# Kernel tuning notes

Hardware: AMD Instinct MI355X
Metric: run time of the kernel (lower is better)

Reference implementation:

```python
import jax, jax.numpy as jnp
import numpy as np


def silu(v):
    return v * jax.nn.sigmoid(v)


def setup_inputs() -> dict:
    key = jax.random.key(0)
    ks = jax.random.split(key, 9)
    B, L, d_model = 2, 2048, 1024
    expand, d_state, d_conv = 2, 16, 4
    d_inner = expand * d_model          # 2048
    dt_rank = (d_model + 15) // 16      # 64 (ceil(d_model/16))
    sc = 0.02
    s = lambda k, shape: (jax.random.normal(k, shape, jnp.float32) * sc)
    A_init = jnp.tile(jnp.arange(1, d_state + 1, dtype=jnp.float32), (d_inner, 1))
    return {
        "x": jax.random.normal(ks[0], (B, L, d_model), jnp.float32),
        "in_proj_w": s(ks[1], (2 * d_inner, d_model)),
        "conv_w": s(ks[2], (d_inner, 1, d_conv)),
        "conv_b": s(ks[3], (d_inner,)),
        "x_proj_w": s(ks[4], (dt_rank + 2 * d_state, d_inner)),
        "dt_proj_w": s(ks[5], (d_inner, dt_rank)),
        "dt_proj_b": s(ks[6], (d_inner,)),
        "A_log": jnp.log(A_init),
        "D": jnp.ones((d_inner,), jnp.float32),
        "out_proj_w": s(ks[7], (d_model, d_inner)),
    }


def _mamba(x, in_proj_w, conv_w, conv_b, x_proj_w, dt_proj_w, dt_proj_b, A_log, D, out_proj_w):
    Bsz, L, d_model = x.shape
    d_inner, _, d_conv = conv_w.shape
    d_state = A_log.shape[1]
    dt_rank = dt_proj_w.shape[1]

    # input projection -> [B, L, 2*d_inner], split into conv branch and gate
    xz = jnp.einsum('bld,ed->ble', x, in_proj_w)
    x_in, z = jnp.split(xz, 2, axis=-1)

    # causal depthwise conv1d over sequence
    xt = jnp.transpose(x_in, (0, 2, 1))                      # [B, d_inner, L]
    xt = jnp.pad(xt, ((0, 0), (0, 0), (d_conv - 1, 0)))
    xc = jax.lax.conv_general_dilated(
        xt, conv_w, window_strides=(1,), padding='VALID',
        dimension_numbers=('NCH', 'OIH', 'NCH'),
        feature_group_count=d_inner)
    xc = xc + conv_b[None, :, None]
    u = silu(jnp.transpose(xc, (0, 2, 1)))                   # [B, L, d_inner]

    # ssm parameter projections
    x_dbl = jnp.einsum('ble,fe->blf', u, x_proj_w)           # [B, L, dt_rank + 2*d_state]
    dt, B_ssm, C_ssm = jnp.split(x_dbl, [dt_rank, dt_rank + d_state], axis=-1)
    delta = jax.nn.softplus(jnp.einsum('blr,er->ble', dt, dt_proj_w) + dt_proj_b)  # [B,L,d_inner]
    A = -jnp.exp(A_log)                                       # [d_inner, d_state]

    # selective scan: h_t = exp(delta_t * A) * h_{t-1} + delta_t * u_t * B_t
    def step(h, inp):
        d_t, B_t, C_t, u_t = inp                              # [B,e],[B,n],[B,n],[B,e]
        dA = jnp.exp(d_t[..., None] * A)                      # [B, d_inner, d_state]
        h = dA * h + (d_t * u_t)[..., None] * B_t[:, None, :]
        y = jnp.einsum('ben,bn->be', h, C_t)
        return h, y

    h0 = jnp.zeros((Bsz, d_inner, d_state), x.dtype)
    scan_in = (jnp.swapaxes(delta, 0, 1), jnp.swapaxes(B_ssm, 0, 1),
               jnp.swapaxes(C_ssm, 0, 1), jnp.swapaxes(u, 0, 1))
    _, ys = jax.lax.scan(step, h0, scan_in)                   # ys: [L, B, d_inner]
    y = jnp.swapaxes(ys, 0, 1) + u * D                        # skip term D*u

    y = y * silu(z)                                           # gate
    return jnp.einsum('ble,de->bld', y, out_proj_w)


def reference(x, in_proj_w, conv_w, conv_b, x_proj_w, dt_proj_w, dt_proj_b, A_log, D, out_proj_w):
    # ResidualMamba: x + Mamba(x)
    return x + _mamba(x, in_proj_w, conv_w, conv_b, x_proj_w,
                      dt_proj_w, dt_proj_b, A_log, D, out_proj_w)
```

## Files before the change

### kernel.cpp

```cpp
#include <hip/hip_runtime.h>
#include <hip/hip_bf16.h>
#include <math.h>

typedef __bf16 bf16;
typedef __attribute__((ext_vector_type(8))) __bf16 bf16x8;
typedef __attribute__((ext_vector_type(4))) __bf16 bf16x4;
typedef __attribute__((ext_vector_type(4))) float  f32x4;

static constexpr int Bsz = 2, L = 2048, DM = 1024, DI = 2048, DS = 16, DTR = 64;
static constexpr int M   = Bsz * L;
static constexpr int NXZ = 2 * DI;
static constexpr int NXD = DTR + 2 * DS;
static constexpr int NC  = 32;
static constexpr int CL  = L / NC;
static constexpr int KS  = 8;
static constexpr float LOG2E = 1.4426950408889634f;

__device__ inline float ex2(float x) { return __builtin_amdgcn_exp2f(x); }

static constexpr int C0 = M * DM / 4;
static constexpr int C1 = C0 + NXZ * DM / 4;
static constexpr int C2 = C1 + DM * DI / 4;
static constexpr int C3 = C2 + NXD * DI / 4;
static constexpr int C4 = C3 + DI * DTR / 4;

__global__ __launch_bounds__(256)
void cast_all(const float* __restrict__ s0, const float* __restrict__ s1,
              const float* __restrict__ s2, const float* __restrict__ s3,
              const float* __restrict__ s4,
              bf16* __restrict__ d0, bf16* __restrict__ d1,
              bf16* __restrict__ d2, bf16* __restrict__ d3,
              bf16* __restrict__ d4)
{
    const int i = blockIdx.x * 256 + threadIdx.x;
    const float* s; bf16* d; int off;
    if      (i < C0) { s = s0; d = d0; off = 0;  }
    else if (i < C1) { s = s1; d = d1; off = C0; }
    else if (i < C2) { s = s2; d = d2; off = C1; }
    else if (i < C3) { s = s3; d = d3; off = C2; }
    else             { s = s4; d = d4; off = C3; }
    const int j = i - off;
    float4 v = ((const float4*)s)[j];
    bf16x4 o = {(bf16)v.x, (bf16)v.y, (bf16)v.z, (bf16)v.w};
    ((bf16x4*)d)[j] = o;
}

__device__ inline void gload_lds16(const void* g, void* l)
{
    __builtin_amdgcn_global_load_lds(
        (const __attribute__((address_space(1))) void*)g,
        (__attribute__((address_space(3))) void*)l, 16, 0, 0);
}

template<int EPI>
__global__ __launch_bounds__(256)
void gemm_bf16(const bf16* __restrict__ A, const bf16* __restrict__ Bw,
               const float* __restrict__ bias, const float* __restrict__ res,
               void* __restrict__ Cout, int N, int K, int lda, int ldc)
{
    __shared__ __align__(16) bf16 Asl[128 * 32];
    __shared__ __align__(16) bf16 Bsl[128 * 32];

    const int tid  = threadIdx.x;
    const int row0 = blockIdx.y * 128;
    const int col0 = blockIdx.x * 128;
    const int w    = tid >> 6;
    const int lane = tid & 63;
    const int wr   = w >> 1, wc = w & 1;
    const int fr   = lane & 15;
    const int ko   = (lane >> 4) << 3;

    f32x4 acc[4][4] = {};

    const int sr = tid >> 2;
    const int sk = (tid & 3) << 3;
    int brow0 = col0 + sr;       if (brow0 > N - 1) brow0 = N - 1;
    int brow1 = col0 + 64 + sr;  if (brow1 > N - 1) brow1 = N - 1;
    const bf16* gA0 = A  + (size_t)(row0 + sr) * lda + sk;
    const bf16* gA1 = A  + (size_t)(row0 + 64 + sr) * lda + sk;
    const bf16* gB0 = Bw + (size_t)brow0 * K + sk;
    const bf16* gB1 = Bw + (size_t)brow1 * K + sk;
    char* lA = (char*)Asl + w * 1024;
    char* lB = (char*)Bsl + w * 1024;

    for (int k0 = 0; k0 < K; k0 += 32) {
        gload_lds16(gA0 + k0, lA);
        gload_lds16(gA1 + k0, lA + 4096);
        gload_lds16(gB0 + k0, lB);
        gload_lds16(gB1 + k0, lB + 4096);
        __syncthreads();

        bf16x8 af[4], bfr[4];
#pragma unroll
        for (int m = 0; m < 4; ++m)
            af[m] = *(const bf16x8*)&Asl[((wr << 6) + m * 16 + fr) * 32 + ko];
#pragma unroll
        for (int n = 0; n < 4; ++n)
            bfr[n] = *(const bf16x8*)&Bsl[((wc << 6) + n * 16 + fr) * 32 + ko];
#pragma unroll
        for (int m = 0; m < 4; ++m)
#pragma unroll
            for (int n = 0; n < 4; ++n)
                acc[m][n] = __builtin_amdgcn_mfma_f32_16x16x32_bf16(
                    af[m], bfr[n], acc[m][n], 0, 0, 0);
        __syncthreads();
    }

    const int r0 = row0 + (wr << 6) + ((lane >> 4) << 2);
    const int c0 = col0 + (wc << 6) + fr;
#pragma unroll
    for (int m = 0; m < 4; ++m) {
#pragma unroll
        for (int n = 0; n < 4; ++n) {
            const int col = c0 + n * 16;
            if (col < N) {
#pragma unroll
                for (int r = 0; r < 4; ++r) {
                    const int row = r0 + m * 16 + r;
                    float v = acc[m][n][r];
                    if (EPI == 0) {
                        ((bf16*)Cout)[(size_t)row * ldc + col] = (bf16)v;
                    } else if (EPI == 1) {
                        v += bias[col];
                        v = (v > 20.f) ? v : log1pf(expf(v));
                        ((bf16*)Cout)[(size_t)row * ldc + col] = (bf16)v;
                    } else {
                        ((float*)Cout)[(size_t)row * ldc + col] =
                            v + res[(size_t)row * ldc + col];
                    }
                }
            }
        }
    }
}

__global__ __launch_bounds__(256)
void gemm_xproj(const bf16* __restrict__ A, const bf16* __restrict__ Bw,
                float* __restrict__ Cpart)
{
    __shared__ __align__(16) bf16 Asl[128 * 32];
    __shared__ __align__(16) bf16 Bsl[128 * 32];

    const int tid  = threadIdx.x;
    const int row0 = blockIdx.x * 128;
    const int kz   = blockIdx.y;
    const int kb   = kz * (2048 / KS);
    const int w    = tid >> 6;
    const int lane = tid & 63;
    const int wr   = w >> 1, wc = w & 1;
    const int fr   = lane & 15;
    const int ko   = (lane >> 4) << 3;

    f32x4 acc[4][4] = {};

    const int sr = tid >> 2;
    const int sk = (tid & 3) << 3;
    int brow0 = sr;       if (brow0 > 95) brow0 = 95;
    int brow1 = 64 + sr;  if (brow1 > 95) brow1 = 95;
    const bf16* gA0 = A  + (size_t)(row0 + sr) * DI + kb + sk;
    const bf16* gA1 = A  + (size_t)(row0 + 64 + sr) * DI + kb + sk;
    const bf16* gB0 = Bw + (size_t)brow0 * DI + kb + sk;
    const bf16* gB1 = Bw + (size_t)brow1 * DI + kb + sk;
    char* lA = (char*)Asl + w * 1024;
    char* lB = (char*)Bsl + w * 1024;

    for (int k0 = 0; k0 < 2048 / KS; k0 += 32) {
        gload_lds16(gA0 + k0, lA);
        gload_lds16(gA1 + k0, lA + 4096);
        gload_lds16(gB0 + k0, lB);
        gload_lds16(gB1 + k0, lB + 4096);
        __syncthreads();

        bf16x8 af[4], bfr[4];
#pragma unroll
        for (int m = 0; m < 4; ++m)
            af[m] = *(const bf16x8*)&Asl[((wr << 6) + m * 16 + fr) * 32 + ko];
#pragma unroll
        for (int n = 0; n < 4; ++n)
            bfr[n] = *(const bf16x8*)&Bsl[((wc << 6) + n * 16 + fr) * 32 + ko];
#pragma unroll
        for (int m = 0; m < 4; ++m)
#pragma unroll
            for (int n = 0; n < 4; ++n)
                acc[m][n] = __builtin_amdgcn_mfma_f32_16x16x32_bf16(
                    af[m], bfr[n], acc[m][n], 0, 0, 0);
        __syncthreads();
    }

    const int r0 = (wr << 6) + ((lane >> 4) << 2);
    const int c0 = (wc << 6) + fr;
    float* Cp = Cpart + (size_t)kz * M * 96 + (size_t)row0 * 96;
#pragma unroll
    for (int m = 0; m < 4; ++m) {
#pragma unroll
        for (int n = 0; n < 4; ++n) {
            const int col = c0 + n * 16;
            if (col < 96) {
#pragma unroll
                for (int r = 0; r < 4; ++r)
                    Cp[(size_t)(r0 + m * 16 + r) * 96 + col] = acc[m][n][r];
            }
        }
    }
}

__global__ __launch_bounds__(256)
void reduce_xdbl(const float* __restrict__ part, bf16* __restrict__ xdb)
{
    const int i = blockIdx.x * 256 + threadIdx.x;
    if (i >= M * 96) return;
    float s = 0.f;
#pragma unroll
    for (int k = 0; k < KS; ++k) s += part[(size_t)k * M * 96 + i];
    xdb[i] = (bf16)s;
}

__global__ __launch_bounds__(256)
void conv_silu(const bf16* __restrict__ xzb, const float* __restrict__ cw,
               const float* __restrict__ cb, bf16* __restrict__ u)
{
    const int idx = blockIdx.x * 256 + threadIdx.x;
    const int e   = (idx & 255) * 8;
    const int m   = idx >> 8;
    const int l   = m & (L - 1);

    float wv[8][4];
#pragma unroll
    for (int c = 0; c < 8; ++c) {
        float4 t = *(const float4*)(cw + (size_t)(e + c) * 4);
        wv[c][0] = t.x; wv[c][1] = t.y; wv[c][2] = t.z; wv[c][3] = t.w;
    }
    float acc[8];
    {
        float4 b0 = *(const float4*)(cb + e);
        float4 b1 = *(const float4*)(cb + e + 4);
        acc[0] = b0.x; acc[1] = b0.y; acc[2] = b0.z; acc[3] = b0.w;
        acc[4] = b1.x; acc[5] = b1.y; acc[6] = b1.z; acc[7] = b1.w;
    }
#pragma unroll
    for (int k = 0; k < 4; ++k) {
        if (l + k - 3 >= 0) {
            bf16x8 xv = *(const bf16x8*)&xzb[(size_t)(m + k - 3) * NXZ + e];
#pragma unroll
            for (int c = 0; c < 8; ++c)
                acc[c] = fmaf((float)xv[c], wv[c][k], acc[c]);
        }
    }
    bf16x8 o;
#pragma unroll
    for (int c = 0; c < 8; ++c)
        o[c] = (bf16)(acc[c] / (1.f + __expf(-acc[c])));
    *(bf16x8*)&u[(size_t)m * DI + e] = o;
}

__global__ __launch_bounds__(256)
void scan_pass1(const bf16* __restrict__ xzb, const bf16* __restrict__ ub,
                const bf16* __restrict__ xdb, const float* __restrict__ A_log,
                float* __restrict__ Pend, float* __restrict__ Qend)
{
    __shared__ bf16 sD[CL][256];
    __shared__ bf16 sU[CL][256];
    __shared__ float Bs[CL][DS];
    const int tid = threadIdx.x;
    const int e0 = blockIdx.x * 256;
    const int e  = e0 + tid;
    const int c = blockIdx.y;
    const int b = blockIdx.z;
    const int l0 = c * CL;

#pragma unroll
    for (int it = 0; it < CL / 8; ++it) {
        const int r   = it * 8 + (tid >> 5);
        const int col = (tid & 31) * 8;
        *(bf16x8*)&sD[r][col] = *(const bf16x8*)&xzb[(size_t)(b * L + l0 + r) * NXZ + e0 + col];
        *(bf16x8*)&sU[r][col] = *(const bf16x8*)&ub [(size_t)(b * L + l0 + r) * DI  + e0 + col];
    }
#pragma unroll
    for (int it = 0; it < CL * DS / 256; ++it) {
        const int idx = it * 256 + tid;
        Bs[idx >> 4][idx & 15] =
            (float)xdb[(size_t)(b * L + l0 + (idx >> 4)) * NXD + DTR + (idx & 15)];
    }

    float A2[DS];
#pragma unroll
    for (int q = 0; q < 4; ++q) {
        float4 al = *(const float4*)(A_log + (size_t)e * DS + q * 4);
        A2[q * 4 + 0] = -__expf(al.x) * LOG2E;
        A2[q * 4 + 1] = -__expf(al.y) * LOG2E;
        A2[q * 4 + 2] = -__expf(al.z) * LOG2E;
        A2[q * 4 + 3] = -__expf(al.w) * LOG2E;
    }

    float h[DS];
#pragma unroll
    for (int n = 0; n < DS; ++n) h[n] = 0.f;
    float sumd = 0.f;

    __syncthreads();

#pragma unroll 4
    for (int t = 0; t < CL; ++t) {
        const float dv = (float)sD[t][tid];
        const float uv = (float)sU[t][tid];
        const float du = dv * uv;
        sumd += dv;
#pragma unroll
        for (int n = 0; n < DS; ++n) {
            const float a = ex2(dv * A2[n]);
            h[n] = fmaf(a, h[n], du * Bs[t][n]);
        }
    }

    const size_t o = ((size_t)(c * Bsz + b) * DI + e) * DS;
#pragma unroll
    for (int q = 0; q < 4; ++q) {
        f32x4 P = {ex2(A2[q*4] * sumd), ex2(A2[q*4+1] * sumd),
                   ex2(A2[q*4+2] * sumd), ex2(A2[q*4+3] * sumd)};
        *(f32x4*)(Pend + o + q * 4) = P;
        *(float4*)(Qend + o + q * 4) = make_float4(h[q*4], h[q*4+1], h[q*4+2], h[q*4+3]);
    }
}

__global__ __launch_bounds__(256)
void scan_pass2(const float* __restrict__ Pend, const float* __restrict__ Qend,
                float* __restrict__ H0)
{
    const int g = blockIdx.x * 256 + threadIdx.x;
    const int stride = Bsz * DI * DS;
    float P[NC], Q[NC];
#pragma unroll
    for (int c = 0; c < NC; ++c) {
        P[c] = Pend[(size_t)c * stride + g];
        Q[c] = Qend[(size_t)c * stride + g];
    }
    float h = 0.f;
#pragma unroll
    for (int c = 0; c < NC; ++c) {
        H0[(size_t)c * stride + g] = h;
        h = fmaf(P[c], h, Q[c]);
    }
}

__global__ __launch_bounds__(256)
void scan_pass3(bf16* __restrict__ xzb, const bf16* __restrict__ ub,
                const bf16* __restrict__ xdb, const float* __restrict__ A_log,
                const float* __restrict__ Dp, const float* __restrict__ H0)
{
    __shared__ bf16 sD[CL][256];
    __shared__ bf16 sU[CL][256];
    __shared__ float BCs[CL][2 * DS];
    const int tid = threadIdx.x;
    const int e0 = blockIdx.x * 256;
    const int e  = e0 + tid;
    const int c = blockIdx.y;
    const int b = blockIdx.z;
    const int l0 = c * CL;

#pragma unroll
    for (int it = 0; it < CL / 8; ++it) {
        const int r   = it * 8 + (tid >> 5);
        const int col = (tid & 31) * 8;
        const size_t grow = (size_t)(b * L + l0 + r);
        *(bf16x8*)&sD[r][col] = *(const bf16x8*)&xzb[grow * NXZ + e0 + col];
        *(bf16x8*)&sU[r][col] = *(const bf16x8*)&ub [grow * DI + e0 + col];
    }
#pragma unroll
    for (int it = 0; it < CL * 2 * DS / 256; ++it) {
        const int idx = it * 256 + tid;
        BCs[idx >> 5][idx & 31] =
            (float)xdb[(size_t)(b * L + l0 + (idx >> 5)) * NXD + DTR + (idx & 31)];
    }

    float A2[DS];
#pragma unroll
    for (int q = 0; q < 4; ++q) {
        float4 al = *(const float4*)(A_log + (size_t)e * DS + q * 4);
        A2[q * 4 + 0] = -__expf(al.x) * LOG2E;
        A2[q * 4 + 1] = -__expf(al.y) * LOG2E;
        A2[q * 4 + 2] = -__expf(al.z) * LOG2E;
        A2[q * 4 + 3] = -__expf(al.w) * LOG2E;
    }

    float h[DS];
    const size_t o = (size_t)c * (Bsz * DI * DS) + ((size_t)b * DI + e) * DS;
#pragma unroll
    for (int q = 0; q < 4; ++q) {
        float4 hv = *(const float4*)(H0 + o + q * 4);
        h[q*4] = hv.x; h[q*4+1] = hv.y; h[q*4+2] = hv.z; h[q*4+3] = hv.w;
    }
    const float Dval = Dp[e];

    __syncthreads();

#pragma unroll 4
    for (int t = 0; t < CL; ++t) {
        const float dv = (float)sD[t][tid];
        const float uv = (float)sU[t][tid];
        const float du = dv * uv;
        float y = 0.f;
#pragma unroll
        for (int n = 0; n < DS; ++n) {
            const float a = ex2(dv * A2[n]);
            h[n] = fmaf(a, h[n], du * BCs[t][n]);
            y = fmaf(h[n], BCs[t][DS + n], y);
        }
        sD[t][tid] = (bf16)(y + uv * Dval);
    }

    __syncthreads();
#pragma unroll
    for (int it = 0; it < CL / 8; ++it) {
        const int r   = it * 8 + (tid >> 5);
        const int col = (tid & 31) * 8;
        const size_t grow = (size_t)(b * L + l0 + r);
        bf16x8 zv = *(const bf16x8*)&xzb[grow * NXZ + DI + e0 + col];
        bf16x8 yv = *(bf16x8*)&sD[r][col];
        bf16x8 ov;
#pragma unroll
        for (int j = 0; j < 8; ++j) {
            const float z = (float)zv[j];
            ov[j] = (bf16)((float)yv[j] * (z / (1.f + __expf(-z))));
        }
        *(bf16x8*)&xzb[grow * NXZ + e0 + col] = ov;
    }
}

extern "C" void kernel_launch(void* const* d_in, const int* in_sizes, int n_in,
                              void* d_out, int out_size, void* d_ws, size_t ws_size,
                              hipStream_t stream)
{
    const float* x          = (const float*)d_in[0];
    const float* in_proj_w  = (const float*)d_in[1];
    const float* conv_w     = (const float*)d_in[2];
    const float* conv_b     = (const float*)d_in[3];
    const float* x_proj_w   = (const float*)d_in[4];
    const float* dt_proj_w  = (const float*)d_in[5];
    const float* dt_proj_b  = (const float*)d_in[6];
    const float* A_log      = (const float*)d_in[7];
    const float* Dp         = (const float*)d_in[8];
    const float* out_proj_w = (const float*)d_in[9];
    float* out = (float*)d_out;

    bf16* xzb   = (bf16*)d_ws;
    bf16* ub    = xzb   + (size_t)M * NXZ;
    bf16* xdb   = ub    + (size_t)M * DI;
    bf16* xb    = xdb   + (size_t)M * NXD;
    bf16* wbin  = xb    + (size_t)M * DM;
    bf16* wbout = wbin  + (size_t)NXZ * DM;
    bf16* wbxp  = wbout + (size_t)DM * DI;
    bf16* wbdt  = wbxp  + (size_t)NXD * DI;
    float* Pend = (float*)(wbdt + (size_t)DI * DTR);
    float* Qend = Pend + (size_t)NC * Bsz * DI * DS;
    float* H0   = Qend + (size_t)NC * Bsz * DI * DS;
    float* xpart = Pend;

    const dim3 blk(256);

    cast_all<<<dim3(C4 / 256), blk, 0, stream>>>(
        x, in_proj_w, out_proj_w, x_proj_w, dt_proj_w,
        xb, wbin, wbout, wbxp, wbdt);

    gemm_bf16<0><<<dim3(NXZ / 128, M / 128), blk, 0, stream>>>(
        xb, wbin, nullptr, nullptr, xzb, NXZ, DM, DM, NXZ);

    conv_silu<<<dim3(M * (DI / 8) / 256), blk, 0, stream>>>(xzb, conv_w, conv_b, ub);

    gemm_xproj<<<dim3(M / 128, KS), blk, 0, stream>>>(ub, wbxp, xpart);
    reduce_xdbl<<<dim3(M * 96 / 256), blk, 0, stream>>>(xpart, xdb);

    gemm_bf16<1><<<dim3(DI / 128, M / 128), blk, 0, stream>>>(
        xdb, wbdt, dt_proj_b, nullptr, xzb, DI, DTR, NXD, NXZ);

    scan_pass1<<<dim3(DI / 256, NC, Bsz), blk, 0, stream>>>(xzb, ub, xdb, A_log, Pend, Qend);
    scan_pass2<<<dim3(Bsz * DI * DS / 256), blk, 0, stream>>>(Pend, Qend, H0);
    scan_pass3<<<dim3(DI / 256, NC, Bsz), blk, 0, stream>>>(xzb, ub, xdb, A_log, Dp, H0);

    gemm_bf16<2><<<dim3(DM / 128, M / 128), blk, 0, stream>>>(
        xzb, wbout, nullptr, x, out, DM, DI, NXZ, DM);
}
```

Baseline: 274.5 us.

## Add 256x256 tiled multi-stage pipelined GEMM for the input projection

Replaces the generic 128x128 bf16 GEMM for the input projection with a dedicated 512-thread kernel. It uses 256x256 tiles, a 4-slot LDS ring buffer filled by direct global-to-LDS loads, XOR-swizzled LDS layout, interleaved prefetch with MFMA phases, s_setprio, and XCD-aware block remapping. The goal is more operand reuse per tile and hiding load latency on the largest GEMM. The cost is one block per CU with heavy register and LDS use, and a hand-tuned waitcnt/barrier schedule that is fragile.

```diff
diff --git a/kernel.cpp b/kernel.cpp
--- a/kernel.cpp
+++ b/kernel.cpp
@@ -17,6 +17,17 @@
 static constexpr float LOG2E = 1.4426950408889634f;
 
 __device__ inline float ex2(float x) { return __builtin_amdgcn_exp2f(x); }
+
+__device__ inline void gload_lds16(const void* g, void* l)
+{
+    __builtin_amdgcn_global_load_lds(
+        (const __attribute__((address_space(1))) void*)g,
+        (__attribute__((address_space(3))) void*)l, 16, 0, 0);
+}
+
+#define SBAR() { asm volatile("" ::: "memory"); __builtin_amdgcn_s_barrier(); asm volatile("" ::: "memory"); }
+#define VMCNT4() asm volatile("s_waitcnt vmcnt(4)" ::: "memory")
+#define VMCNT0() asm volatile("s_waitcnt vmcnt(0)" ::: "memory")
 
 static constexpr int C0 = M * DM / 4;
 static constexpr int C1 = C0 + NXZ * DM / 4;
@@ -45,11 +56,142 @@
     ((bf16x4*)d)[j] = o;
 }
 
-__device__ inline void gload_lds16(const void* g, void* l)
-{
-    __builtin_amdgcn_global_load_lds(
-        (const __attribute__((address_space(1))) void*)g,
-        (__attribute__((address_space(3))) void*)l, 16, 0, 0);
+static constexpr int GK  = DM;
+static constexpr int GNT = GK / 64;
+
+__device__ __forceinline__ void stage_half(const bf16* __restrict__ Gbase, int ld,
+                                           int kbase, bf16* lds_slot, int tid, int wid)
+{
+    const int rl = tid >> 2;
+    const int ks = ((tid & 3) ^ (rl & 3)) << 3;
+#pragma unroll
+    for (int i = 0; i < 2; ++i)
+        gload_lds16(Gbase + (size_t)(i * 128 + rl) * ld + kbase + ks,
+                    lds_slot + i * 4096 + wid * 512);
+}
+
+template<int MH>
+__device__ __forceinline__ void ldA4(const bf16* As, int abase, bf16x8 af[4])
+{
+#pragma unroll
+    for (int mm = 0; mm < 4; ++mm)
+        af[mm] = *(const bf16x8*)(As + abase + (MH * 4 + mm) * 512);
+}
+
+__device__ __forceinline__ void ldB4(const bf16* Bs, int bbase, bf16x8 bfr[4])
+{
+#pragma unroll
+    for (int nn = 0; nn < 4; ++nn)
+        bfr[nn] = *(const bf16x8*)(Bs + bbase + nn * 512);
+}
+
+template<int MH>
+__device__ __forceinline__ void mfma16(f32x4 acc[8][4], const bf16x8 af[4],
+                                       const bf16x8 bfr[4])
+{
+#pragma unroll
+    for (int mm = 0; mm < 4; ++mm)
+#pragma unroll
+        for (int nn = 0; nn < 4; ++nn)
+            acc[MH * 4 + mm][nn] = __builtin_amdgcn_mfma_f32_16x16x32_bf16(
+                af[mm], bfr[nn], acc[MH * 4 + mm][nn], 0, 0, 0);
+}
+
+__global__ __launch_bounds__(512, 1)
+void gemm256_inproj(const bf16* __restrict__ A, const bf16* __restrict__ Bw,
+                    bf16* __restrict__ C)
+{
+    __shared__ __align__(16) bf16 Asl[4 * 8192];
+    __shared__ __align__(16) bf16 Bsl[4 * 8192];
+
+    const int tid  = threadIdx.x;
+    const int wid  = tid >> 6;
+    const int lane = tid & 63;
+    const int wr   = wid >> 2;
+    const int wc   = wid & 3;
+    const int fr   = lane & 15;
+    const int ko16 = lane >> 4;
+    const int kx   = ((ko16 ^ (fr & 3)) << 3);
+
+    const int bid = blockIdx.x;
+    const int wg  = (bid & 7) * 32 + (bid >> 3);
+    const int by  = wg >> 4, bx = wg & 15;
+    const int row0 = by * 256, col0 = bx * 256;
+
+    const bf16* Ablk = A  + (size_t)row0 * GK;
+    const bf16* Bblk = Bw + (size_t)col0 * GK;
+
+    const int abase = (wr * 128 + fr) * 32 + kx;
+    const int bbase = (wc * 64 + fr) * 32 + kx;
+
+    f32x4 acc[8][4] = {};
+    bf16x8 af[4], bfr[4];
+
+    stage_half(Ablk, GK, 0,       Asl + 0 * 8192, tid, wid);
+    stage_half(Bblk, GK, 0,       Bsl + 0 * 8192, tid, wid);
+    stage_half(Ablk, GK, 32,      Asl + 1 * 8192, tid, wid);
+    stage_half(Bblk, GK, 32,      Bsl + 1 * 8192, tid, wid);
+    stage_half(Ablk, GK, 64,      Asl + 2 * 8192, tid, wid);
+    stage_half(Bblk, GK, 64,      Bsl + 2 * 8192, tid, wid);
+    VMCNT4();
+    SBAR();
+
+    for (int t = 0; t < GNT; ++t) {
+        const int sk0 = (2 * t) & 3, sk1 = (2 * t + 1) & 3;
+        const bf16* As0 = Asl + sk0 * 8192;
+        const bf16* As1 = Asl + sk1 * 8192;
+        const bf16* Bs0 = Bsl + sk0 * 8192;
+        const bf16* Bs1 = Bsl + sk1 * 8192;
+
+        ldA4<0>(As0, abase, af);
+        ldB4(Bs0, bbase, bfr);
+        if (t + 1 < GNT)
+            stage_half(Ablk, GK, (t + 1) * 64 + 32, Asl + ((2 * t + 3) & 3) * 8192, tid, wid);
+        SBAR();
+        __builtin_amdgcn_s_setprio(1);
+        mfma16<0>(acc, af, bfr);
+        __builtin_amdgcn_s_setprio(0);
+        SBAR();
+
+        ldA4<1>(As0, abase, af);
+        if (t + 1 < GNT)
+            stage_half(Bblk, GK, (t + 1) * 64 + 32, Bsl + ((2 * t + 3) & 3) * 8192, tid, wid);
+        SBAR();
+        __builtin_amdgcn_s_setprio(1);
+        mfma16<1>(acc, af, bfr);
+        __builtin_amdgcn_s_setprio(0);
+        SBAR();
+
+        ldA4<0>(As1, abase, af);
+        ldB4(Bs1, bbase, bfr);
+        if (t + 2 < GNT)
+            stage_half(Ablk, GK, (t + 2) * 64, Asl + sk0 * 8192, tid, wid);
+        SBAR();
+        __builtin_amdgcn_s_setprio(1);
+        mfma16<0>(acc, af, bfr);
+        __builtin_amdgcn_s_setprio(0);
+        SBAR();
+
+        ldA4<1>(As1, abase, af);
+        if (t + 2 < GNT)
+            stage_half(Bblk, GK, (t + 2) * 64, Bsl + sk0 * 8192, tid, wid);
+        SBAR();
+        __builtin_amdgcn_s_setprio(1);
+        mfma16<1>(acc, af, bfr);
+        __builtin_amdgcn_s_setprio(0);
+        if (t < GNT - 3) { VMCNT4(); } else { VMCNT0(); }
+        SBAR();
+    }
+
+    const int r0 = row0 + wr * 128 + (ko16 << 2);
+    const int c0 = col0 + wc * 64 + fr;
+#pragma unroll
+    for (int m = 0; m < 8; ++m)
+#pragma unroll
+        for (int n = 0; n < 4; ++n)
+#pragma unroll
+            for (int r = 0; r < 4; ++r)
+                C[(size_t)(r0 + m * 16 + r) * NXZ + c0 + n * 16] = (bf16)acc[m][n][r];
 }
 
 template<int EPI>
@@ -461,8 +603,7 @@
         x, in_proj_w, out_proj_w, x_proj_w, dt_proj_w,
         xb, wbin, wbout, wbxp, wbdt);
 
-    gemm_bf16<0><<<dim3(NXZ / 128, M / 128), blk, 0, stream>>>(
-        xb, wbin, nullptr, nullptr, xzb, NXZ, DM, DM, NXZ);
+    gemm256_inproj<<<dim3(256), dim3(512), 0, stream>>>(xb, wbin, xzb);
 
     conv_silu<<<dim3(M * (DI / 8) / 256), blk, 0, stream>>>(xzb, conv_w, conv_b, ub);
 
```

Result: faster. 261.3 us (-4.8%).
